# Optimization experiments

Measured on AMD Instinct MI355X. Metric: run time of the kernel, lower is better.

Reference implementation:

```python
import jax, jax.numpy as jnp
import numpy as np

C_IN = 2048
C_HID = 1024
C_EMB = 256


def setup_inputs() -> dict:
    key = jax.random.key(0)
    ks = jax.random.split(key, 14)
    B, T = 4, 2048
    sc = 0.02  # keep logits in a sane range for softmax
    inp = {
        "x": jax.random.normal(ks[0], (B, T, C_IN), jnp.float32) * 0.05,
        "theta_w": jax.random.normal(ks[1], (C_HID, C_IN), jnp.float32) * sc,
        "theta_b": jnp.zeros((C_HID,), jnp.float32),
        "phi_w": jax.random.normal(ks[2], (C_HID, C_IN), jnp.float32) * sc,
        "phi_b": jnp.zeros((C_HID,), jnp.float32),
        "g_w": jax.random.normal(ks[3], (C_HID, C_IN), jnp.float32) * sc,
        "g_b": jnp.zeros((C_HID,), jnp.float32),
        "rou_w": jax.random.normal(ks[4], (2,), jnp.float32),
        "rou_b": jnp.zeros((1,), jnp.float32),
        "w_w": jax.random.normal(ks[5], (C_IN, C_HID), jnp.float32) * sc,
        "w_b": jnp.zeros((C_IN,), jnp.float32),
        "emb_w": jax.random.normal(ks[6], (C_EMB, C_IN), jnp.float32) * sc,
        "emb_b": jnp.zeros((C_EMB,), jnp.float32),
        "B": B,
        "T": T,
    }
    return inp


def reference(x, theta_w, theta_b, phi_w, phi_b, g_w, g_b, rou_w, rou_b,
              w_w, w_b, emb_w, emb_b, B, T):
    x = x.reshape(B, T, C_IN)
    # NSSM: raw self-similarity + softmax over last dim -> (B, T, T)
    nssm = jax.nn.softmax(jnp.einsum('btc,bsc->bts', x, x), axis=-1)
    xc = jnp.swapaxes(x, 1, 2)  # (B, C_IN, T), channels-first like Conv1d
    # 1x1 Conv1d == per-timestep linear over channels
    x_theta = jnp.einsum('oc,bct->bot', theta_w, xc) + theta_b[None, :, None]  # (B,H,T)
    x_phi = jnp.einsum('oc,bct->bto', phi_w, xc) + phi_b[None, None, :]        # (B,T,H)
    att = jax.nn.softmax(jnp.einsum('bth,bhs->bts', x_phi, x_theta), axis=-1)  # (B,T,T)
    # Faithful to torch.cat(dim=0).view(B,-1,T,T): row-major interleave of batches
    cat = jnp.concatenate([nssm, att], axis=0).reshape(B, 2, T, T)
    # rou: 1x1 Conv2d(2->1) == weighted sum of the two maps + bias, then softmax
    moca = jax.nn.softmax(rou_w[0] * cat[:, 0] + rou_w[1] * cat[:, 1] + rou_b[0], axis=-1)  # (B,T,T)
    x_g = jnp.einsum('oc,bct->bot', g_w, xc) + g_b[None, :, None]  # (B,H,T)
    y = jnp.einsum('bht,bts->bhs', x_g, moca)                      # (B,H,T)
    wz = jnp.einsum('oh,bht->bot', w_w, y) + w_b[None, :, None]    # (B,C_IN,T)
    z = jnp.swapaxes(wz + xc, 1, 2)                                # (B,T,C_IN)
    return z @ emb_w.T + emb_b                                     # (B,T,256)
```

## Files before the change

kernel.cpp:

```cpp
#include <hip/hip_runtime.h>
#include <hip/hip_bf16.h>

constexpr int kB   = 4;
constexpr int kT   = 2048;
constexpr int kCIN = 2048;
constexpr int kHID = 1024;
constexpr int kEMB = 256;

typedef __bf16 bf16_t;
typedef __bf16 bf16x8 __attribute__((ext_vector_type(8)));
typedef __bf16 bf16x4 __attribute__((ext_vector_type(4)));
typedef float  f32x4  __attribute__((ext_vector_type(4)));

__device__ __forceinline__ void gll16(const void* g, void* l) {
  auto lp = reinterpret_cast<__attribute__((address_space(3))) uint32_t*>(
      reinterpret_cast<uintptr_t>(l));
  __builtin_amdgcn_global_load_lds(static_cast<const uint32_t*>(g), lp, 16, 0, 0);
}

#define MFMA_BF16 __builtin_amdgcn_mfma_f32_16x16x32_bf16

template <int MODE>
__device__ __forceinline__ void gemm256(bf16_t* lds, const bf16_t* A, const bf16_t* B,
                                        void* Cv, int lda, int ldb, int ldc,
                                        int m0, int n0, int Klen, const float* biasN) {
  const int tid  = threadIdx.x;
  const int lane = tid & 63, wv = tid >> 6;
  const int wm = wv & 1, wn = wv >> 1;
  const int lm = lane & 15, q = lane >> 4;
  const int l8 = lane >> 3;
  const int slot = (lane & 7) ^ l8;

  bf16_t* const sA = lds;
  bf16_t* const sB = lds + 32768;

  int aoff[4], boff[4];
#pragma unroll
  for (int cc = 0; cc < 4; cc++) {
    const int ra = cc * 64 + wv * 8 + l8;
    aoff[cc] = ra * lda;
    const int nb = ((ra >> 5) & 3) * 64 + (ra >> 7) * 32 + (ra & 31);
    boff[cc] = nb * ldb;
  }
  const bf16_t* const Ab = A + (size_t)m0 * lda + slot * 8;
  const bf16_t* const Bb = B + (size_t)n0 * ldb + slot * 8;

  const int x0 = ((q ^ (lm & 7)) << 3);
  const int x1 = (((q + 4) ^ (lm & 7)) << 3);

#define STAGE_A(T, H)                                                         \
  {                                                                           \
    bf16_t* dst_ = sA + (((T) & 1) << 14);                                    \
    const bf16_t* src_ = Ab + ((T) << 6);                                     \
    gll16(src_ + aoff[(H)], dst_ + ((H) << 12) + (wv << 9));                  \
    gll16(src_ + aoff[2 + (H)], dst_ + ((2 + (H)) << 12) + (wv << 9));        \
  }
#define STAGE_B(T, G)                                                         \
  {                                                                           \
    bf16_t* dst_ = sB + (((T) & 1) << 14);                                    \
    const bf16_t* src_ = Bb + ((T) << 6);                                     \
    gll16(src_ + boff[2 * (G)], dst_ + ((2 * (G)) << 12) + (wv << 9));        \
    gll16(src_ + boff[2 * (G) + 1], dst_ + ((2 * (G) + 1) << 12) + (wv << 9));\
  }
#define READ_A(BUF, H)                                                        \
  _Pragma("unroll") for (int i = 0; i < 4; i++) {                             \
    const bf16_t* p_ = (BUF) + ((wm * 128 + (H) * 64 + i * 16 + lm) << 6);    \
    af[i][0] = *(const bf16x8*)(p_ + x0);                                     \
    af[i][1] = *(const bf16x8*)(p_ + x1);                                     \
  }
#define READ_B(BF, BUF, G)                                                    \
  _Pragma("unroll") for (int j2 = 0; j2 < 2; j2++) {                          \
    const bf16_t* p_ = (BUF) + (((G) * 128 + wn * 32 + j2 * 16 + lm) << 6);   \
    BF[j2][0] = *(const bf16x8*)(p_ + x0);                                    \
    BF[j2][1] = *(const bf16x8*)(p_ + x1);                                    \
  }
#define QUAD(H, G, BF)                                                        \
  _Pragma("unroll") for (int i2 = 0; i2 < 4; i2++)                            \
  _Pragma("unroll") for (int j2 = 0; j2 < 2; j2++)                            \
  _Pragma("unroll") for (int kk = 0; kk < 2; kk++)                            \
    acc[(H) * 4 + i2][(G) * 2 + j2] = MFMA_BF16(                              \
        af[i2][kk], BF[j2][kk], acc[(H) * 4 + i2][(G) * 2 + j2], 0, 0, 0);
#define MFMA_OPEN()                                                           \
  asm volatile("s_waitcnt lgkmcnt(0)" ::: "memory");                          \
  __builtin_amdgcn_s_setprio(1);
#define MFMA_CLOSE() __builtin_amdgcn_s_setprio(0);

  f32x4 acc[8][4];
#pragma unroll
  for (int i = 0; i < 8; i++)
#pragma unroll
    for (int j = 0; j < 4; j++)
#pragma unroll
      for (int r = 0; r < 4; r++) acc[i][j][r] = 0.f;

  const int nt = Klen >> 6;

  STAGE_A(0, 0) STAGE_B(0, 0) STAGE_B(0, 1) STAGE_A(0, 1)
  STAGE_A(1, 0) STAGE_B(1, 0) STAGE_B(1, 1) STAGE_A(1, 1)
  asm volatile("s_waitcnt vmcnt(8)" ::: "memory");
  __builtin_amdgcn_s_barrier();

  bf16x8 af[4][2], bf0[2][2], bf1[2][2];
  for (int t = 0; t < nt; t++) {
    bf16_t* const a = sA + ((t & 1) << 14);
    bf16_t* const b = sB + ((t & 1) << 14);
    const bool pf = (t + 2) < nt;
    READ_A(a, 0)
    READ_B(bf0, b, 0)
    asm volatile("s_waitcnt lgkmcnt(8)" ::: "memory");
    __builtin_amdgcn_s_barrier();
    MFMA_OPEN()
    QUAD(0, 0, bf0)
    MFMA_CLOSE()
    __builtin_amdgcn_s_barrier();
    READ_B(bf1, b, 1)
    if (pf) STAGE_A(t + 2, 0)
    __builtin_amdgcn_s_barrier();
    MFMA_OPEN()
    QUAD(0, 1, bf1)
    MFMA_CLOSE()
    __builtin_amdgcn_s_barrier();
    READ_A(a, 1)
    if (pf) STAGE_B(t + 2, 0)
    __builtin_amdgcn_s_barrier();
    MFMA_OPEN()
    QUAD(1, 1, bf1)
    MFMA_CLOSE()
    __builtin_amdgcn_s_barrier();
    if (pf) { STAGE_B(t + 2, 1) STAGE_A(t + 2, 1) }
    __builtin_amdgcn_s_barrier();
    __builtin_amdgcn_s_setprio(1);
    QUAD(1, 0, bf0)
    __builtin_amdgcn_s_setprio(0);
    if (pf)
      asm volatile("s_waitcnt vmcnt(8)" ::: "memory");
    else if (t + 1 < nt)
      asm volatile("s_waitcnt vmcnt(0)" ::: "memory");
    __builtin_amdgcn_s_barrier();
  }

#pragma unroll
  for (int i = 0; i < 8; i++) {
    const int gm = m0 + wm * 128 + (i >> 2) * 64 + (i & 3) * 16 + q * 4;
#pragma unroll
    for (int j = 0; j < 4; j++) {
      const int gn = n0 + wn * 64 + j * 16 + lm;
      const float bn_ = biasN ? biasN[gn] : 0.f;
#pragma unroll
      for (int r = 0; r < 4; r++) {
        const float v = acc[i][j][r] + bn_;
        const size_t idx = (size_t)(gm + r) * ldc + gn;
        if (MODE == 0)      ((bf16_t*)Cv)[idx] = (bf16_t)v;
        else if (MODE == 1) ((float*)Cv)[idx] = v;
        else                atomicAdd(&((float*)Cv)[idx], v);
      }
    }
  }
#undef STAGE_A
#undef STAGE_B
#undef READ_A
#undef READ_B
#undef QUAD
#undef MFMA_OPEN
#undef MFMA_CLOSE
}

__global__ __launch_bounds__(256) void k_prep(const float* __restrict__ x,
                                              const float* __restrict__ th,
                                              const float* __restrict__ ph,
                                              const float* __restrict__ g,
                                              const float* __restrict__ emb,
                                              const float* __restrict__ w_w,
                                              const float* __restrict__ w_b,
                                              const float* __restrict__ emb_b,
                                              const float* __restrict__ tb,
                                              const float* __restrict__ pb,
                                              const float* __restrict__ gb,
                                              bf16_t* __restrict__ xbf,
                                              bf16_t* __restrict__ wqkv,
                                              bf16_t* __restrict__ embbf,
                                              bf16_t* __restrict__ wwT,
                                              float* __restrict__ biase,
                                              float* __restrict__ bqkv,
                                              float* __restrict__ out) {
  __shared__ float tile[64 * 66];
  const int b = blockIdx.x;
  if (b < 23040) {
    const float* in; bf16_t* o; long i;
    if (b < 16384)      { in = x;   o = xbf;                            i = (long)b * 256 + threadIdx.x; }
    else if (b < 18432) { in = th;  o = wqkv;                           i = (long)(b - 16384) * 256 + threadIdx.x; }
    else if (b < 20480) { in = ph;  o = wqkv + (size_t)kHID * kCIN;     i = (long)(b - 18432) * 256 + threadIdx.x; }
    else if (b < 22528) { in = g;   o = wqkv + (size_t)2 * kHID * kCIN; i = (long)(b - 20480) * 256 + threadIdx.x; }
    else                { in = emb; o = embbf;                          i = (long)(b - 22528) * 256 + threadIdx.x; }
    float4 v = ((const float4*)in)[i];
    bf16x4 ov;
    ov[0] = (bf16_t)v.x; ov[1] = (bf16_t)v.y; ov[2] = (bf16_t)v.z; ov[3] = (bf16_t)v.w;
    ((bf16x4*)o)[i] = ov;
  } else if (b < 23552) {
    int j = b - 23040;
    int h0 = (j & 15) * 64, c0 = (j >> 4) * 64;
#pragma unroll
    for (int k = 0; k < 16; k++) {
      int e = k * 256 + threadIdx.x;
      int r = e >> 6, c = e & 63;
      tile[r * 66 + c] = w_w[(size_t)(c0 + r) * kHID + h0 + c];
    }
    __syncthreads();
#pragma unroll
    for (int k = 0; k < 16; k++) {
      int e = k * 256 + threadIdx.x;
      int r = e >> 6, c = e & 63;
      wwT[(size_t)(h0 + r) * kCIN + c0 + c] = (bf16_t)tile[c * 66 + r];
    }
  } else if (b < 23808) {
    int e = b - 23552;
    float acc = 0.f;
    for (int c = threadIdx.x; c < kCIN; c += 256)
      acc += emb[(size_t)e * kCIN + c] * w_b[c];
#pragma unroll
    for (int o = 32; o > 0; o >>= 1) acc += __shfl_xor(acc, o, 64);
    __syncthreads();
    if ((threadIdx.x & 63) == 0) tile[threadIdx.x >> 6] = acc;
    __syncthreads();
    if (threadIdx.x == 0) biase[e] = tile[0] + tile[1] + tile[2] + tile[3] + emb_b[e];
  } else if (b < 23820) {
    int i = (b - 23808) * 256 + threadIdx.x;
    if (i < 3072)
      bqkv[i] = i < 1024 ? tb[i] : (i < 2048 ? pb[i - 1024] : gb[i - 2048]);
  } else {
    long i = (long)(b - 23820) * 256 + threadIdx.x;
    ((float4*)out)[i] = make_float4(0.f, 0.f, 0.f, 0.f);
  }
}

__global__ __launch_bounds__(512, 2) void k_mega1(const bf16_t* __restrict__ xbf,
                                                  const bf16_t* __restrict__ wqkv,
                                                  const bf16_t* __restrict__ embbf,
                                                  const bf16_t* __restrict__ wwT,
                                                  bf16_t* __restrict__ xtphi,
                                                  bf16_t* __restrict__ S1,
                                                  bf16_t* __restrict__ Mbf,
                                                  const float* __restrict__ bqkv,
                                                  float* __restrict__ S1f) {
  __shared__ bf16_t lds[65536];
  const int bid = blockIdx.x;
  if (bid < 384) {
    const int bm = bid & 31, bn = bid >> 5;
    gemm256<0>(lds, xbf, wqkv, xtphi, 2048, 2048, 3072,
               bm * 256, bn * 256, 2048, bqkv);
  } else if (bid < 508) {
    int s = bid - 384;
    const int z = s / 36;
    int tt = s % 36, rr = 0;
    while (tt >= 8 - rr) { tt -= 8 - rr; rr++; }
    const bf16_t* Az = xbf + (size_t)z * kT * kCIN;
    gemm256<0>(lds, Az, Az, S1 + (size_t)z * kT * kT, 2048, 2048, 2048,
               rr * 256, (rr + tt) * 256, 2048, nullptr);
  } else if (bid < 512) {
    const int m = bid - 508;
    gemm256<0>(lds, embbf, wwT, Mbf, 2048, 2048, 1024, 0, m * 256, 2048, nullptr);
  } else {
    const int qj = bid - 512;
    const int s = 124 + (qj >> 2), ks = qj & 3;
    const int z = s / 36;
    int tt = s % 36, rr = 0;
    while (tt >= 8 - rr) { tt -= 8 - rr; rr++; }
    const bf16_t* Az = xbf + (size_t)z * kT * kCIN;
    gemm256<1>(lds, Az + (size_t)(rr * 256) * 2048 + ks * 512,
               Az + (size_t)((rr + tt) * 256) * 2048 + ks * 512,
               S1f + (size_t)qj * 65536, 2048, 2048, 256, 0, 0, 512, nullptr);
  }
}

__global__ __launch_bounds__(512, 2) void k_gemm2(const bf16_t* __restrict__ xtphi,
                                                  bf16_t* __restrict__ S2,
                                                  const float* __restrict__ S1f,
                                                  bf16_t* __restrict__ S1) {
  __shared__ bf16_t lds[65536];
  const int bid = blockIdx.x;
  if (bid < 256) {
    const int bm = bid & 7, bn = (bid >> 3) & 7, z = bid >> 6;
    const bf16_t* base = xtphi + (size_t)z * kT * 3072;
    gemm256<0>(lds, base + 1024, base, S2 + (size_t)z * kT * kT, 3072, 3072, 2048,
               bm * 256, bn * 256, 1024, nullptr);
    return;
  }
  const int cb = bid - 256;
  const int t20 = cb >> 4, part = cb & 15;
  const int s = 124 + t20;
  const int z = s / 36;
  int tt = s % 36, rr = 0;
  while (tt >= 8 - rr) { tt -= 8 - rr; rr++; }
  const float* base = S1f + (size_t)(4 * t20) * 65536;
  const int e0 = part * 4096 + threadIdx.x * 8;
  f32x4 lo = *(const f32x4*)(base + e0) ;
  f32x4 hi = *(const f32x4*)(base + e0 + 4);
#pragma unroll
  for (int ks = 1; ks < 4; ks++) {
    const float* p = base + (size_t)ks * 65536 + e0;
    f32x4 l2 = *(const f32x4*)p, h2 = *(const f32x4*)(p + 4);
#pragma unroll
    for (int k = 0; k < 4; k++) { lo[k] += l2[k]; hi[k] += h2[k]; }
  }
  const int r = e0 >> 8, c = e0 & 255;
  bf16x8 o;
#pragma unroll
  for (int k = 0; k < 4; k++) { o[k] = (bf16_t)lo[k]; o[4 + k] = (bf16_t)hi[k]; }
  *(bf16x8*)(S1 + (size_t)z * kT * kT + (size_t)(rr * 256 + r) * kT + (rr + tt) * 256 + c) = o;
}

__global__ __launch_bounds__(256) void k_util(bf16_t* __restrict__ S1,
                                              const bf16_t* __restrict__ xtphi,
                                              bf16_t* __restrict__ xgT) {
  __shared__ bf16_t tile[64 * 66];
  const int bid = blockIdx.x;
  const size_t T2 = (size_t)kT * kT;
  if (bid < 1984) {
    int z = bid / 496, t = bid % 496, qq = 0;
    while (t >= 31 - qq) { t -= 31 - qq; qq++; }
    int p = qq + 1 + t;
    const size_t base = (size_t)z * T2;
#pragma unroll
    for (int k = 0; k < 16; k++) {
      int e = k * 256 + threadIdx.x;
      int r = e >> 6, c = e & 63;
      tile[r * 66 + c] = S1[base + (size_t)(qq * 64 + r) * kT + p * 64 + c];
    }
    __syncthreads();
#pragma unroll
    for (int k = 0; k < 16; k++) {
      int e = k * 256 + threadIdx.x;
      int r = e >> 6, c = e & 63;
      S1[base + (size_t)(p * 64 + r) * kT + qq * 64 + c] = tile[c * 66 + r];
    }
  } else {
    int j = bid - 1984;
    int hb = j & 15, tb2 = (j >> 4) & 31, z = j >> 9;
#pragma unroll
    for (int k = 0; k < 16; k++) {
      int e = k * 256 + threadIdx.x;
      int r = e >> 6, c = e & 63;
      tile[r * 66 + c] = xtphi[(size_t)(z * kT + tb2 * 64 + r) * 3072 + 2048 + hb * 64 + c];
    }
    __syncthreads();
#pragma unroll
    for (int k = 0; k < 16; k++) {
      int e = k * 256 + threadIdx.x;
      int r = e >> 6, c = e & 63;
      xgT[(size_t)z * kHID * kT + (size_t)(hb * 64 + r) * kT + tb2 * 64 + c] = tile[c * 66 + r];
    }
  }
}

__global__ __launch_bounds__(256) void k_moca(const bf16_t* __restrict__ S1,
                                              const bf16_t* __restrict__ S2,
                                              bf16_t* __restrict__ dst,
                                              const float* __restrict__ rou_w,
                                              const float* __restrict__ rou_b) {
  const int wv = threadIdx.x >> 6, lane = threadIdx.x & 63;
  const int t = blockIdx.x * 4 + wv, b = blockIdx.y;
  const size_t T2 = (size_t)kT * kT;
  const bf16_t* src = (b < 2) ? S1 : S2;
  const int pb = (b < 2) ? 2 * b : 2 * (b - 2);
  const bf16_t* rA = src + (size_t)pb * T2 + (size_t)t * kT;
  const bf16_t* rB = rA + T2;

  float va[32], vb[32];
#pragma unroll
  for (int c = 0; c < 4; c++) {
    bf16x8 a  = *(const bf16x8*)(rA + c * 512 + lane * 8);
    bf16x8 bb = *(const bf16x8*)(rB + c * 512 + lane * 8);
#pragma unroll
    for (int k = 0; k < 8; k++) { va[c * 8 + k] = (float)a[k]; vb[c * 8 + k] = (float)bb[k]; }
  }
  auto wmax = [](float v) {
#pragma unroll
    for (int o = 32; o > 0; o >>= 1) v = fmaxf(v, __shfl_xor(v, o, 64));
    return v;
  };
  auto wsum = [](float v) {
#pragma unroll
    for (int o = 32; o > 0; o >>= 1) v += __shfl_xor(v, o, 64);
    return v;
  };

  float m = -1e30f, s;
#pragma unroll
  for (int j = 0; j < 32; j++) m = fmaxf(m, va[j]);
  m = wmax(m); s = 0.f;
#pragma unroll
  for (int j = 0; j < 32; j++) { va[j] = __expf(va[j] - m); s += va[j]; }
  const float invA = 1.f / wsum(s);

  m = -1e30f;
#pragma unroll
  for (int j = 0; j < 32; j++) m = fmaxf(m, vb[j]);
  m = wmax(m); s = 0.f;
#pragma unroll
  for (int j = 0; j < 32; j++) { vb[j] = __expf(vb[j] - m); s += vb[j]; }
  const float invB = 1.f / wsum(s);

  const float r0 = rou_w[0], r1 = rou_w[1], rb2 = rou_b[0];
#pragma unroll
  for (int j = 0; j < 32; j++) va[j] = r0 * va[j] * invA + r1 * vb[j] * invB + rb2;

  m = -1e30f;
#pragma unroll
  for (int j = 0; j < 32; j++) m = fmaxf(m, va[j]);
  m = wmax(m); s = 0.f;
#pragma unroll
  for (int j = 0; j < 32; j++) { va[j] = __expf(va[j] - m); s += va[j]; }
  const float invC = 1.f / wsum(s);

  bf16_t* o = dst + (size_t)b * T2 + (size_t)t * kT;
#pragma unroll
  for (int c = 0; c < 4; c++) {
    bf16x8 ov;
#pragma unroll
    for (int k = 0; k < 8; k++) ov[k] = (bf16_t)(va[c * 8 + k] * invC);
    *(bf16x8*)(o + c * 512 + lane * 8) = ov;
  }
}

__global__ __launch_bounds__(256) void k_mocaT(const bf16_t* __restrict__ in,
                                               bf16_t* __restrict__ out) {
  __shared__ bf16_t tile[64 * 66];
  size_t base = (size_t)blockIdx.z * kT * kT;
  int r0 = blockIdx.y * 64, c0 = blockIdx.x * 64;
#pragma unroll
  for (int k = 0; k < 16; k++) {
    int e = k * 256 + threadIdx.x;
    int r = e >> 6, c = e & 63;
    tile[r * 66 + c] = in[base + (size_t)(r0 + r) * kT + c0 + c];
  }
  __syncthreads();
#pragma unroll
  for (int k = 0; k < 16; k++) {
    int e = k * 256 + threadIdx.x;
    int r = e >> 6, c = e & 63;
    out[base + (size_t)(c0 + r) * kT + r0 + c] = tile[c * 66 + r];
  }
}

__global__ __launch_bounds__(512, 2) void k_tail1(const bf16_t* __restrict__ mocaT,
                                                  const bf16_t* __restrict__ xgT,
                                                  bf16_t* __restrict__ yT,
                                                  const bf16_t* __restrict__ xbf,
                                                  const bf16_t* __restrict__ embbf,
                                                  float* __restrict__ out,
                                                  const float* __restrict__ biase) {
  __shared__ bf16_t lds[65536];
  const int bid = blockIdx.x;
  if (bid < 128) {
    const int bm = bid & 7, bn = (bid >> 3) & 3, z = bid >> 5;
    gemm256<0>(lds, mocaT + (size_t)z * kT * kT, xgT + (size_t)z * kHID * kT,
               yT + (size_t)z * kT * kHID, 2048, 2048, 1024,
               bm * 256, bn * 256, 2048, nullptr);
  } else {
    const int r = bid - 128;
    const int bm = r & 31, ks = r >> 5;
    gemm256<2>(lds, xbf + ks * 512, embbf + ks * 512, out, 2048, 2048, 256,
               bm * 256, 0, 512, ks == 0 ? biase : nullptr);
  }
}

__global__ __launch_bounds__(512, 2) void k_tail2(const bf16_t* __restrict__ yT,
                                                  const bf16_t* __restrict__ Mbf,
                                                  float* __restrict__ out) {
  __shared__ bf16_t lds[65536];
  const int bid = blockIdx.x;
  const int bm = bid & 31, ks = bid >> 5;
  gemm256<2>(lds, yT + ks * 256, Mbf + ks * 256, out, 1024, 1024, 256,
             bm * 256, 0, 256, nullptr);
}

extern "C" void kernel_launch(void* const* d_in, const int* in_sizes, int n_in,
                              void* d_out, int out_size, void* d_ws, size_t ws_size,
                              hipStream_t stream) {
  const float* x       = (const float*)d_in[0];
  const float* theta_w = (const float*)d_in[1];
  const float* theta_b = (const float*)d_in[2];
  const float* phi_w   = (const float*)d_in[3];
  const float* phi_b   = (const float*)d_in[4];
  const float* g_w     = (const float*)d_in[5];
  const float* g_b     = (const float*)d_in[6];
  const float* rou_w   = (const float*)d_in[7];
  const float* rou_b   = (const float*)d_in[8];
  const float* w_w     = (const float*)d_in[9];
  const float* w_b     = (const float*)d_in[10];
  const float* emb_w   = (const float*)d_in[11];
  const float* emb_b   = (const float*)d_in[12];
  float* out = (float*)d_out;

  char* ws = (char*)d_ws;
  size_t off = 0;
  auto alloc = [&](size_t bytes) -> char* {
    off = (off + 255) & ~(size_t)255;
    char* p = ws + off;
    off += bytes;
    return p;
  };

  const size_t BT = (size_t)kB * kT;
  const size_t T2 = (size_t)kT * kT;

  bf16_t* xbf   = (bf16_t*)alloc(BT * kCIN * 2);
  bf16_t* wqkv  = (bf16_t*)alloc((size_t)3 * kHID * kCIN * 2);
  bf16_t* embbf = (bf16_t*)alloc((size_t)kEMB * kCIN * 2);
  bf16_t* wwT   = (bf16_t*)alloc((size_t)kHID * kCIN * 2);
  bf16_t* xtphi = (bf16_t*)alloc(BT * 3072 * 2);
  bf16_t* xgT   = (bf16_t*)alloc((size_t)kB * kHID * kT * 2);
  bf16_t* mocab = (bf16_t*)alloc((size_t)kB * T2 * 2);
  bf16_t* Mbf   = (bf16_t*)alloc((size_t)kEMB * kHID * 2);
  float*  biase = (float*)alloc((size_t)kEMB * 4);
  float*  bqkv  = (float*)alloc((size_t)3072 * 4);
  bf16_t* S1    = (bf16_t*)alloc((size_t)kB * T2 * 2);
  bf16_t* S2    = (bf16_t*)alloc((size_t)kB * T2 * 2);
  bf16_t* mocaT = (bf16_t*)xtphi;
  bf16_t* yT    = (bf16_t*)S2;
  float*  S1f   = (float*)mocab;

  k_prep<<<dim3(25868), 256, 0, stream>>>(x, theta_w, phi_w, g_w, emb_w, w_w, w_b,
                                          emb_b, theta_b, phi_b, g_b,
                                          xbf, wqkv, embbf, wwT, biase, bqkv, out);
  k_mega1<<<dim3(592), 512, 0, stream>>>(xbf, wqkv, embbf, wwT, xtphi, S1, Mbf,
                                         bqkv, S1f);
  k_gemm2<<<dim3(576), 512, 0, stream>>>(xtphi, S2, S1f, S1);
  k_util<<<dim3(4032), 256, 0, stream>>>(S1, xtphi, xgT);
  k_moca<<<dim3(kT / 4, kB), 256, 0, stream>>>(S1, S2, mocab, rou_w, rou_b);
  k_mocaT<<<dim3(32, 32, kB), 256, 0, stream>>>(mocab, mocaT);
  k_tail1<<<dim3(256), 512, 0, stream>>>(mocaT, xgT, yT, xbf, embbf, out, biase);
  k_tail2<<<dim3(128), 512, 0, stream>>>(yT, Mbf, out);
}
```

Baseline: 456.2 us.

## Reassociate output chain to fold emb·W·g into per-batch W before moca GEMM

Precomputes W = (emb·w_w)·x_g per batch, a 256×T matrix, so the final stage multiplies moca by a 256-row operand instead of computing the 1024-row y and then projecting it. This removes the large moca×x_g GEMM and the x_g transpose. Atomic accumulation into out is replaced by split-K partial buffers plus a reduction kernel that adds the bias, which also removes the zero-fill of out. S1 mirror-transpose tiles are moved partly into the gemm2 launch to fill idle slots. The cost is extra fp32 scratch traffic and a different bf16 rounding order.

```diff
diff --git a/kernel.cpp b/kernel.cpp
--- a/kernel.cpp
+++ b/kernel.cpp
@@ -150,9 +150,8 @@
       for (int r = 0; r < 4; r++) {
         const float v = acc[i][j][r] + bn_;
         const size_t idx = (size_t)(gm + r) * ldc + gn;
-        if (MODE == 0)      ((bf16_t*)Cv)[idx] = (bf16_t)v;
-        else if (MODE == 1) ((float*)Cv)[idx] = v;
-        else                atomicAdd(&((float*)Cv)[idx], v);
+        if (MODE == 0) ((bf16_t*)Cv)[idx] = (bf16_t)v;
+        else           ((float*)Cv)[idx] = v;
       }
     }
   }
@@ -163,6 +162,12 @@
 #undef QUAD
 #undef MFMA_OPEN
 #undef MFMA_CLOSE
+}
+
+__device__ __forceinline__ bool mirror_is_late(int z, int qq, int p) {
+  const int R = qq >> 2, C = p >> 2;
+  const int local = 8 * R - (R * (R - 1)) / 2 + (C - R);
+  return (z == 3) && (local >= 16);
 }
 
 __global__ __launch_bounds__(256) void k_prep(const float* __restrict__ x,
@@ -181,8 +186,7 @@
                                               bf16_t* __restrict__ embbf,
                                               bf16_t* __restrict__ wwT,
                                               float* __restrict__ biase,
-                                              float* __restrict__ bqkv,
-                                              float* __restrict__ out) {
+                                              float* __restrict__ bqkv) {
   __shared__ float tile[64 * 66];
   const int b = blockIdx.x;
   if (b < 23040) {
@@ -223,13 +227,10 @@
     if ((threadIdx.x & 63) == 0) tile[threadIdx.x >> 6] = acc;
     __syncthreads();
     if (threadIdx.x == 0) biase[e] = tile[0] + tile[1] + tile[2] + tile[3] + emb_b[e];
-  } else if (b < 23820) {
+  } else {
     int i = (b - 23808) * 256 + threadIdx.x;
     if (i < 3072)
       bqkv[i] = i < 1024 ? tb[i] : (i < 2048 ? pb[i - 1024] : gb[i - 2048]);
-  } else {
-    long i = (long)(b - 23820) * 256 + threadIdx.x;
-    ((float4*)out)[i] = make_float4(0.f, 0.f, 0.f, 0.f);
   }
 }
 
@@ -275,7 +276,9 @@
 __global__ __launch_bounds__(512, 2) void k_gemm2(const bf16_t* __restrict__ xtphi,
                                                   bf16_t* __restrict__ S2,
                                                   const float* __restrict__ S1f,
-                                                  bf16_t* __restrict__ S1) {
+                                                  bf16_t* __restrict__ S1,
+                                                  const bf16_t* __restrict__ Mbf,
+                                                  float* __restrict__ Wf) {
   __shared__ bf16_t lds[65536];
   const int bid = blockIdx.x;
   if (bid < 256) {
@@ -283,43 +286,73 @@
     const bf16_t* base = xtphi + (size_t)z * kT * 3072;
     gemm256<0>(lds, base + 1024, base, S2 + (size_t)z * kT * kT, 3072, 3072, 2048,
                bm * 256, bn * 256, 1024, nullptr);
-    return;
-  }
-  const int cb = bid - 256;
-  const int t20 = cb >> 4, part = cb & 15;
-  const int s = 124 + t20;
-  const int z = s / 36;
-  int tt = s % 36, rr = 0;
-  while (tt >= 8 - rr) { tt -= 8 - rr; rr++; }
-  const float* base = S1f + (size_t)(4 * t20) * 65536;
-  const int e0 = part * 4096 + threadIdx.x * 8;
-  f32x4 lo = *(const f32x4*)(base + e0) ;
-  f32x4 hi = *(const f32x4*)(base + e0 + 4);
-#pragma unroll
-  for (int ks = 1; ks < 4; ks++) {
-    const float* p = base + (size_t)ks * 65536 + e0;
-    f32x4 l2 = *(const f32x4*)p, h2 = *(const f32x4*)(p + 4);
-#pragma unroll
-    for (int k = 0; k < 4; k++) { lo[k] += l2[k]; hi[k] += h2[k]; }
-  }
-  const int r = e0 >> 8, c = e0 & 255;
-  bf16x8 o;
-#pragma unroll
-  for (int k = 0; k < 4; k++) { o[k] = (bf16_t)lo[k]; o[4 + k] = (bf16_t)hi[k]; }
-  *(bf16x8*)(S1 + (size_t)z * kT * kT + (size_t)(rr * 256 + r) * kT + (rr + tt) * 256 + c) = o;
-}
-
-__global__ __launch_bounds__(256) void k_util(bf16_t* __restrict__ S1,
-                                              const bf16_t* __restrict__ xtphi,
-                                              bf16_t* __restrict__ xgT) {
+  } else if (bid < 320) {
+    const int wj = bid - 256;
+    const int tle = wj & 31, ks = wj >> 5;
+    const int z = tle >> 3, ntile = tle & 7;
+    gemm256<1>(lds, Mbf + ks * 512,
+               xtphi + (size_t)(z * kT + ntile * 256) * 3072 + 2048 + ks * 512,
+               Wf + (size_t)(ks * 32 + tle) * 65536, 1024, 3072, 256, 0, 0, 512,
+               nullptr);
+  } else if (bid < 640) {
+    const int cb = bid - 320;
+    const int t20 = cb >> 4, part = cb & 15;
+    const int s = 124 + t20;
+    const int z = s / 36;
+    int tt = s % 36, rr = 0;
+    while (tt >= 8 - rr) { tt -= 8 - rr; rr++; }
+    const float* base = S1f + (size_t)(4 * t20) * 65536;
+    const int e0 = part * 4096 + threadIdx.x * 8;
+    f32x4 lo = *(const f32x4*)(base + e0);
+    f32x4 hi = *(const f32x4*)(base + e0 + 4);
+#pragma unroll
+    for (int ks = 1; ks < 4; ks++) {
+      const float* p = base + (size_t)ks * 65536 + e0;
+      f32x4 l2 = *(const f32x4*)p, h2 = *(const f32x4*)(p + 4);
+#pragma unroll
+      for (int k = 0; k < 4; k++) { lo[k] += l2[k]; hi[k] += h2[k]; }
+    }
+    const int r = e0 >> 8, c = e0 & 255;
+    bf16x8 o;
+#pragma unroll
+    for (int k = 0; k < 4; k++) { o[k] = (bf16_t)lo[k]; o[4 + k] = (bf16_t)hi[k]; }
+    *(bf16x8*)(S1 + (size_t)z * kT * kT + (size_t)(rr * 256 + r) * kT + (rr + tt) * 256 + c) = o;
+  } else {
+    int j = bid - 640;
+    int z = j / 496, t = j % 496, qq = 0;
+    while (t >= 31 - qq) { t -= 31 - qq; qq++; }
+    int p = qq + 1 + t;
+    if (mirror_is_late(z, qq, p)) return;
+    bf16_t* tile = lds;
+    const size_t base = (size_t)z * kT * kT;
+#pragma unroll
+    for (int k = 0; k < 8; k++) {
+      int e = k * 512 + threadIdx.x;
+      int r = e >> 6, c = e & 63;
+      tile[r * 66 + c] = S1[base + (size_t)(qq * 64 + r) * kT + p * 64 + c];
+    }
+    __syncthreads();
+#pragma unroll
+    for (int k = 0; k < 8; k++) {
+      int e = k * 512 + threadIdx.x;
+      int r = e >> 6, c = e & 63;
+      S1[base + (size_t)(p * 64 + r) * kT + qq * 64 + c] = tile[c * 66 + r];
+    }
+  }
+}
+
+__global__ __launch_bounds__(256) void k_util2(bf16_t* __restrict__ S1,
+                                               const float* __restrict__ Wf,
+                                               bf16_t* __restrict__ W) {
   __shared__ bf16_t tile[64 * 66];
   const int bid = blockIdx.x;
-  const size_t T2 = (size_t)kT * kT;
   if (bid < 1984) {
-    int z = bid / 496, t = bid % 496, qq = 0;
+    int j = bid;
+    int z = j / 496, t = j % 496, qq = 0;
     while (t >= 31 - qq) { t -= 31 - qq; qq++; }
     int p = qq + 1 + t;
-    const size_t base = (size_t)z * T2;
+    if (!mirror_is_late(z, qq, p)) return;
+    const size_t base = (size_t)z * kT * kT;
 #pragma unroll
     for (int k = 0; k < 16; k++) {
       int e = k * 256 + threadIdx.x;
@@ -334,21 +367,20 @@
       S1[base + (size_t)(p * 64 + r) * kT + qq * 64 + c] = tile[c * 66 + r];
     }
   } else {
-    int j = bid - 1984;
-    int hb = j & 15, tb2 = (j >> 4) & 31, z = j >> 9;
-#pragma unroll
-    for (int k = 0; k < 16; k++) {
-      int e = k * 256 + threadIdx.x;
-      int r = e >> 6, c = e & 63;
-      tile[r * 66 + c] = xtphi[(size_t)(z * kT + tb2 * 64 + r) * 3072 + 2048 + hb * 64 + c];
-    }
-    __syncthreads();
-#pragma unroll
-    for (int k = 0; k < 16; k++) {
-      int e = k * 256 + threadIdx.x;
-      int r = e >> 6, c = e & 63;
-      xgT[(size_t)z * kHID * kT + (size_t)(hb * 64 + r) * kT + tb2 * 64 + c] = tile[c * 66 + r];
-    }
+    const long i = (long)(bid - 1984) * 2048 + threadIdx.x * 8;
+    const int tle = (int)(i >> 16), w = (int)(i & 65535);
+    const float* a = Wf + (size_t)tle * 65536 + w;
+    const float* b = a + (size_t)32 * 65536;
+    f32x4 lo = *(const f32x4*)a, hi = *(const f32x4*)(a + 4);
+    f32x4 l2 = *(const f32x4*)b, h2 = *(const f32x4*)(b + 4);
+    const int e = w >> 8, sl = w & 255;
+    bf16x8 o;
+#pragma unroll
+    for (int k = 0; k < 4; k++) {
+      o[k]     = (bf16_t)(lo[k] + l2[k]);
+      o[4 + k] = (bf16_t)(hi[k] + h2[k]);
+    }
+    *(bf16x8*)(W + (size_t)(tle >> 3) * kEMB * kT + (size_t)e * kT + (tle & 7) * 256 + sl) = o;
   }
 }
 
@@ -442,36 +474,49 @@
   }
 }
 
-__global__ __launch_bounds__(512, 2) void k_tail1(const bf16_t* __restrict__ mocaT,
-                                                  const bf16_t* __restrict__ xgT,
-                                                  bf16_t* __restrict__ yT,
-                                                  const bf16_t* __restrict__ xbf,
-                                                  const bf16_t* __restrict__ embbf,
-                                                  float* __restrict__ out,
-                                                  const float* __restrict__ biase) {
+__global__ __launch_bounds__(512, 2) void k_outq(const bf16_t* __restrict__ mocaT,
+                                                 const bf16_t* __restrict__ W,
+                                                 const bf16_t* __restrict__ xbf,
+                                                 const bf16_t* __restrict__ embbf,
+                                                 float* __restrict__ outf) {
   __shared__ bf16_t lds[65536];
   const int bid = blockIdx.x;
-  if (bid < 128) {
-    const int bm = bid & 7, bn = (bid >> 3) & 3, z = bid >> 5;
-    gemm256<0>(lds, mocaT + (size_t)z * kT * kT, xgT + (size_t)z * kHID * kT,
-               yT + (size_t)z * kT * kHID, 2048, 2048, 1024,
-               bm * 256, bn * 256, 2048, nullptr);
+  const int m = bid & 31, ks = bid >> 5;
+  float* Cv = outf + (size_t)ks * 2097152 + (size_t)m * 65536;
+  if (ks < 4) {
+    const int z = m >> 3;
+    gemm256<1>(lds,
+               mocaT + (size_t)z * kT * kT + (size_t)((m & 7) * 256) * kT + ks * 512,
+               W + (size_t)z * kEMB * kT + ks * 512,
+               Cv, 2048, 2048, 256, 0, 0, 512, nullptr);
   } else {
-    const int r = bid - 128;
-    const int bm = r & 31, ks = r >> 5;
-    gemm256<2>(lds, xbf + ks * 512, embbf + ks * 512, out, 2048, 2048, 256,
-               bm * 256, 0, 512, ks == 0 ? biase : nullptr);
-  }
-}
-
-__global__ __launch_bounds__(512, 2) void k_tail2(const bf16_t* __restrict__ yT,
-                                                  const bf16_t* __restrict__ Mbf,
-                                                  float* __restrict__ out) {
-  __shared__ bf16_t lds[65536];
-  const int bid = blockIdx.x;
-  const int bm = bid & 31, ks = bid >> 5;
-  gemm256<2>(lds, yT + ks * 256, Mbf + ks * 256, out, 1024, 1024, 256,
-             bm * 256, 0, 256, nullptr);
+    gemm256<1>(lds,
+               xbf + (size_t)(m * 256) * kCIN + (ks - 4) * 512,
+               embbf + (ks - 4) * 512,
+               Cv, 2048, 2048, 256, 0, 0, 512, nullptr);
+  }
+}
+
+__global__ __launch_bounds__(256) void k_fin(const float* __restrict__ outf,
+                                             const float* __restrict__ biase,
+                                             float* __restrict__ out) {
+  const long i = (long)blockIdx.x * 2048 + threadIdx.x * 8;
+  const int e0 = (int)(i & 255);
+  f32x4 lo = {0.f, 0.f, 0.f, 0.f}, hi = {0.f, 0.f, 0.f, 0.f};
+#pragma unroll
+  for (int ks = 0; ks < 8; ks++) {
+    const float* p = outf + (size_t)ks * 2097152 + i;
+    f32x4 l2 = *(const f32x4*)p, h2 = *(const f32x4*)(p + 4);
+#pragma unroll
+    for (int k = 0; k < 4; k++) { lo[k] += l2[k]; hi[k] += h2[k]; }
+  }
+#pragma unroll
+  for (int k = 0; k < 4; k++) {
+    lo[k] += biase[e0 + k];
+    hi[k] += biase[e0 + 4 + k];
+  }
+  *(f32x4*)(out + i) = lo;
+  *(f32x4*)(out + i + 4) = hi;
 }
 
 extern "C" void kernel_launch(void* const* d_in, const int* in_sizes, int n_in,
@@ -509,26 +554,27 @@
   bf16_t* embbf = (bf16_t*)alloc((size_t)kEMB * kCIN * 2);
   bf16_t* wwT   = (bf16_t*)alloc((size_t)kHID * kCIN * 2);
   bf16_t* xtphi = (bf16_t*)alloc(BT * 3072 * 2);
-  bf16_t* xgT   = (bf16_t*)alloc((size_t)kB * kHID * kT * 2);
+  float*  Wf    = (float*)alloc((size_t)64 * 65536 * 4);
   bf16_t* mocab = (bf16_t*)alloc((size_t)kB * T2 * 2);
   bf16_t* Mbf   = (bf16_t*)alloc((size_t)kEMB * kHID * 2);
+  bf16_t* W     = (bf16_t*)alloc((size_t)kB * kEMB * kT * 2);
   float*  biase = (float*)alloc((size_t)kEMB * 4);
   float*  bqkv  = (float*)alloc((size_t)3072 * 4);
   bf16_t* S1    = (bf16_t*)alloc((size_t)kB * T2 * 2);
   bf16_t* S2    = (bf16_t*)alloc((size_t)kB * T2 * 2);
   bf16_t* mocaT = (bf16_t*)xtphi;
-  bf16_t* yT    = (bf16_t*)S2;
   float*  S1f   = (float*)mocab;
-
-  k_prep<<<dim3(25868), 256, 0, stream>>>(x, theta_w, phi_w, g_w, emb_w, w_w, w_b,
+  float*  outf  = (float*)S1;
+
+  k_prep<<<dim3(23820), 256, 0, stream>>>(x, theta_w, phi_w, g_w, emb_w, w_w, w_b,
                                           emb_b, theta_b, phi_b, g_b,
-                                          xbf, wqkv, embbf, wwT, biase, bqkv, out);
+                                          xbf, wqkv, embbf, wwT, biase, bqkv);
   k_mega1<<<dim3(592), 512, 0, stream>>>(xbf, wqkv, embbf, wwT, xtphi, S1, Mbf,
                                          bqkv, S1f);
-  k_gemm2<<<dim3(576), 512, 0, stream>>>(xtphi, S2, S1f, S1);
-  k_util<<<dim3(4032), 256, 0, stream>>>(S1, xtphi, xgT);
+  k_gemm2<<<dim3(2624), 512, 0, stream>>>(xtphi, S2, S1f, S1, Mbf, Wf);
+  k_util2<<<dim3(3008), 256, 0, stream>>>(S1, Wf, W);
   k_moca<<<dim3(kT / 4, kB), 256, 0, stream>>>(S1, S2, mocab, rou_w, rou_b);
   k_mocaT<<<dim3(32, 32, kB), 256, 0, stream>>>(mocab, mocaT);
-  k_tail1<<<dim3(256), 512, 0, stream>>>(mocaT, xgT, yT, xbf, embbf, out, biase);
-  k_tail2<<<dim3(128), 512, 0, stream>>>(yT, Mbf, out);
-}
+  k_outq<<<dim3(256), 512, 0, stream>>>(mocaT, W, xbf, embbf, outf);
+  k_fin<<<dim3(1024), 256, 0, stream>>>(outf, biase, out);
+}
```

Result: faster. 416.7 us (-8.7%).
